# Performance work log

Measured on AMD Instinct MI355X. Metric: run time of the kernel, lower is better.

Reference implementation:

```python
import jax, jax.numpy as jnp
import numpy as np

B, T, D, K = 64, 276, 256, 8192


def setup_inputs() -> dict:
    key = jax.random.key(0)
    k1, k2 = jax.random.split(key)
    z = jax.random.normal(k1, (B, T, D), dtype=jnp.float32)
    # nn.Embedding weight init: uniform(-1/K, 1/K)
    codebook = jax.random.uniform(k2, (K, D), dtype=jnp.float32,
                                  minval=-1.0 / K, maxval=1.0 / K)
    return {"z": z, "codebook": codebook}


def reference(z, codebook):
    """Faithful port of X_BERT_VQVAE.quantize.

    z: [B, T, D] encoder output; codebook: [K, D].
    Returns (loss_vq, loss_commit, z_q [B,T,D] with straight-through, min_idx [B,T]).
    """
    bsz, t, dim = z.shape
    zf = z.reshape(bsz * t, dim)                       # (b t) d
    # pairwise sq-dist: ||z||^2 + ||c||^2 - 2 z.c  -> [(b t), K]
    d = (jnp.sum(zf * zf, axis=1, keepdims=True)
         + jnp.sum(codebook * codebook, axis=1)
         - 2.0 * zf @ codebook.T)
    min_idx = jnp.argmin(d, axis=1)                    # [(b t)]
    z_q = codebook[min_idx]                            # [(b t), D] gather
    loss_vq = jnp.mean((z_q - jax.lax.stop_gradient(zf)) ** 2)
    loss_commit = jnp.mean((zf - jax.lax.stop_gradient(z_q)) ** 2)
    # straight-through estimator
    z_q_st = zf + jax.lax.stop_gradient(z_q - zf)
    return (loss_vq, loss_commit,
            z_q_st.reshape(bsz, t, dim),
            min_idx.reshape(bsz, t))
```

## Files before the change

### kernel.cpp

```cpp
#include <hip/hip_runtime.h>
#include <hip/hip_bf16.h>

#define M_ROWS 17664
#define K_CODES 8192
#define D_DIM 256
#define N_ELEM 4521984

typedef unsigned short ushort_t;
typedef __attribute__((ext_vector_type(8))) short short8v;
typedef __attribute__((ext_vector_type(4))) float f32x4;

__device__ __forceinline__ unsigned long long umin64(unsigned long long a, unsigned long long b) { return a < b ? a : b; }

__device__ __forceinline__ unsigned long long shflxor64(unsigned long long v, int m) {
    unsigned lo = (unsigned)v, hi = (unsigned)(v >> 32);
    lo = __shfl_xor(lo, m);
    hi = __shfl_xor(hi, m);
    return ((unsigned long long)hi << 32) | lo;
}

__device__ __forceinline__ void gload16(const void* g, void* l) {
    __builtin_amdgcn_global_load_lds((const __attribute__((address_space(1))) void*)g,
                                     (__attribute__((address_space(3))) void*)l, 16, 0, 0);
}

__global__ __launch_bounds__(256) void prep_kernel(
    const float* __restrict__ Z, const float* __restrict__ CB,
    ushort_t* __restrict__ Zb, ushort_t* __restrict__ Cb,
    float* __restrict__ asum, float* __restrict__ bsum,
    float* __restrict__ loss_acc) {
    __shared__ float S[32][257];
    const int t = threadIdx.x;
    const int bid = blockIdx.x;
    const float* X; ushort_t* Xb; float* sums; int r0;
    if (bid < M_ROWS / 32) { X = Z; Xb = Zb; sums = asum; r0 = bid * 32; }
    else { X = CB; Xb = Cb; sums = bsum; r0 = (bid - M_ROWS / 32) * 32; }
    if (bid == 0 && t == 0) loss_acc[0] = 0.0f;
#pragma unroll
    for (int it = 0; it < 8; ++it) {
        int idx4 = t + it * 256;
        int row = idx4 >> 6;
        int c4 = (idx4 & 63) * 4;
        const float4 v = *(const float4*)(X + (size_t)(r0 + row) * D_DIM + c4);
        float vv[4] = {v.x, v.y, v.z, v.w};
        ushort_t h[4];
#pragma unroll
        for (int j = 0; j < 4; ++j) {
            __hip_bfloat16 b = __float2bfloat16(vv[j]);
            h[j] = *reinterpret_cast<ushort_t*>(&b);
        }
        *(ushort4*)(Xb + (size_t)(r0 + row) * D_DIM + c4) =
            make_ushort4(h[0], h[1], h[2], h[3]);
        S[row][c4 + 0] = v.x; S[row][c4 + 1] = v.y;
        S[row][c4 + 2] = v.z; S[row][c4 + 3] = v.w;
    }
    __syncthreads();
    if (t < 32) {
        float half_sum[2];
#pragma unroll
        for (int h = 0; h < 2; ++h) {
            const float* q = &S[t][h * 128];
            float acc[8];
#pragma unroll
            for (int j = 0; j < 8; ++j) acc[j] = __fmul_rn(q[j], q[j]);
            for (int i = 8; i < 128; i += 8) {
#pragma unroll
                for (int j = 0; j < 8; ++j)
                    acc[j] = __fadd_rn(acc[j], __fmul_rn(q[i + j], q[i + j]));
            }
            float s01 = __fadd_rn(acc[0], acc[1]);
            float s23 = __fadd_rn(acc[2], acc[3]);
            float s45 = __fadd_rn(acc[4], acc[5]);
            float s67 = __fadd_rn(acc[6], acc[7]);
            half_sum[h] = __fadd_rn(__fadd_rn(s01, s23), __fadd_rn(s45, s67));
        }
        sums[r0 + t] = __fadd_rn(half_sum[0], half_sum[1]);
    }
}

__global__ __launch_bounds__(256, 4) void phase1_kernel(
    const ushort_t* __restrict__ Zb,
    const ushort_t* __restrict__ Cb,
    const float* __restrict__ bsum,
    unsigned* __restrict__ blockcand) {
    __shared__ ushort_t As[8192];
    __shared__ ushort_t Bs[8192];

    const int t = threadIdx.x;
    const int wid = t >> 6, lane = t & 63;
    const int wm = wid >> 1, wn = wid & 1;

    const int bid = blockIdx.x;
    const int bn = ((bid & 7) << 3) + ((bid >> 3) & 7);
    const int bm = bid >> 6;
    const int m0 = bm * 128, n0 = bn * 128;

    f32x4 acc[4][4];
#pragma unroll
    for (int i = 0; i < 4; ++i)
#pragma unroll
        for (int jj = 0; jj < 4; ++jj) acc[i][jj] = (f32x4){0.f, 0.f, 0.f, 0.f};

    const int srow8 = t >> 3;
    const int sslot = t & 7;
    const int srcq = (sslot ^ (srow8 & 7)) * 8;
    const ushort_t* zsrc = Zb + (size_t)(m0 + srow8) * 256 + srcq;
    const ushort_t* csrc = Cb + (size_t)(n0 + srow8) * 256 + srcq;
    const int dst0 = srow8 * 64 + sslot * 8;

    const int fr = lane & 15, q = lane >> 4;
    const int ph0 = (q ^ (fr & 7)) * 8;
    const int ph1 = ((4 + q) ^ (fr & 7)) * 8;

#pragma unroll
    for (int i = 0; i < 4; ++i) {
        gload16(zsrc + (size_t)i * 8192, &As[dst0 + i * 2048]);
        gload16(csrc + (size_t)i * 8192, &Bs[dst0 + i * 2048]);
    }

#pragma unroll
    for (int c = 0; c < 4; ++c) {
        asm volatile("s_waitcnt vmcnt(0)" ::: "memory");
        __builtin_amdgcn_s_barrier();
        asm volatile("" ::: "memory");

        short8v a0[4], b0[4];
#pragma unroll
        for (int mi = 0; mi < 4; ++mi)
            a0[mi] = *(const short8v*)(&Bs[(wn * 64 + mi * 16 + fr) * 64 + ph0]);
#pragma unroll
        for (int nj = 0; nj < 4; ++nj)
            b0[nj] = *(const short8v*)(&As[(wm * 64 + nj * 16 + fr) * 64 + ph0]);
        __builtin_amdgcn_s_setprio(1);
#pragma unroll
        for (int mi = 0; mi < 4; ++mi)
#pragma unroll
            for (int nj = 0; nj < 4; ++nj)
                acc[mi][nj] = __builtin_amdgcn_mfma_f32_16x16x32_bf16(
                    a0[mi], b0[nj], acc[mi][nj], 0, 0, 0);
        __builtin_amdgcn_s_setprio(0);

        short8v a1[4], b1[4];
#pragma unroll
        for (int mi = 0; mi < 4; ++mi)
            a1[mi] = *(const short8v*)(&Bs[(wn * 64 + mi * 16 + fr) * 64 + ph1]);
#pragma unroll
        for (int nj = 0; nj < 4; ++nj)
            b1[nj] = *(const short8v*)(&As[(wm * 64 + nj * 16 + fr) * 64 + ph1]);
        asm volatile("s_waitcnt lgkmcnt(0)" ::: "memory");
        __builtin_amdgcn_sched_barrier(0);
        __builtin_amdgcn_s_barrier();
        asm volatile("" ::: "memory");

        if (c < 3) {
            const int kc = (c + 1) * 64;
#pragma unroll
            for (int i = 0; i < 4; ++i) {
                gload16(zsrc + (size_t)i * 8192 + kc, &As[dst0 + i * 2048]);
                gload16(csrc + (size_t)i * 8192 + kc, &Bs[dst0 + i * 2048]);
            }
        }

        __builtin_amdgcn_s_setprio(1);
#pragma unroll
        for (int mi = 0; mi < 4; ++mi)
#pragma unroll
            for (int nj = 0; nj < 4; ++nj)
                acc[mi][nj] = __builtin_amdgcn_mfma_f32_16x16x32_bf16(
                    a1[mi], b1[nj], acc[mi][nj], 0, 0, 0);
        __builtin_amdgcn_s_setprio(0);
    }

    unsigned* cand = (unsigned*)&As[0];
    const int colb = n0 + wn * 64 + q * 4;
    float bc16[16];
#pragma unroll
    for (int mi = 0; mi < 4; ++mi)
#pragma unroll
        for (int r = 0; r < 4; ++r)
            bc16[mi * 4 + r] = bsum[colb + mi * 16 + r];

    const float INF = __uint_as_float(0x7f800000u);
#pragma unroll
    for (int nj = 0; nj < 4; ++nj) {
        float m1 = INF, m2 = INF;
#pragma unroll
        for (int mi = 0; mi < 4; ++mi)
#pragma unroll
            for (int r = 0; r < 4; ++r) {
                float dm = __builtin_fmaf(-2.0f, acc[mi][nj][r], bc16[mi * 4 + r]);
                unsigned e = (__float_as_uint(dm) & 0xFFFFE000u) |
                             (unsigned)(colb + mi * 16 + r);
                float fe = __uint_as_float(e);
                m2 = __builtin_amdgcn_fmed3f(m1, m2, fe);
                m1 = fminf(m1, fe);
            }
#pragma unroll
        for (int s = 16; s <= 32; s <<= 1) {
            float o1 = __shfl_xor(m1, s);
            float o2 = __shfl_xor(m2, s);
            float nm2 = fminf(fmaxf(m1, o1), fminf(m2, o2));
            m1 = fminf(m1, o1);
            m2 = nm2;
        }
        if (q == 0) {
            int zr = wm * 64 + nj * 16 + fr;
            cand[zr * 9 + wn * 2 + 0] = __float_as_uint(m1);
            cand[zr * 9 + wn * 2 + 1] = __float_as_uint(m2);
        }
    }
    __syncthreads();
    if (t < 128) {
        float b1 = INF, b2 = INF;
#pragma unroll
        for (int j = 0; j < 4; ++j) {
            float f = __uint_as_float(cand[t * 9 + j]);
            b2 = __builtin_amdgcn_fmed3f(b1, b2, f);
            b1 = fminf(b1, f);
        }
        *(uint2*)(blockcand + (size_t)(m0 + t) * 128 + bn * 2) =
            make_uint2(__float_as_uint(b1), __float_as_uint(b2));
    }
}

__global__ __launch_bounds__(256) void phase2_kernel(
    const float* __restrict__ Z, const float* __restrict__ CB,
    const float* __restrict__ asum, const float* __restrict__ bsum,
    const unsigned* __restrict__ blockcand,
    float* __restrict__ out, float* __restrict__ loss_acc) {
    float* out_zq = out + 2;
    float* out_idx = out + 2 + (size_t)N_ELEM;
    const int lane = threadIdx.x & 63;
    const int w = threadIdx.x >> 6;
    const int gw = blockIdx.x * 4 + w;
    const int NW = M_ROWS / 4;
    float lsum = 0.0f;

    int row = gw;
    uint2 E = *(const uint2*)(blockcand + (size_t)row * 128 + lane * 2);
    float4 zv = *(const float4*)(Z + (size_t)row * D_DIM + lane * 4);
    float ar = asum[row];

#pragma unroll 1
    for (int it = 0; it < 4; ++it) {
        const int nrow = row + NW;
        uint2 En = E; float4 zvn = zv; float arn = ar;
        if (it < 3) {
            En = *(const uint2*)(blockcand + (size_t)nrow * 128 + lane * 2);
            zvn = *(const float4*)(Z + (size_t)nrow * D_DIM + lane * 4);
            arn = asum[nrow];
        }

        float f0 = __uint_as_float(E.x), f1 = __uint_as_float(E.y);
        float mn = fminf(f0, f1);
#pragma unroll
        for (int s = 1; s < 64; s <<= 1) mn = fminf(mn, __shfl_xor(mn, s));
        const float thr = mn + 5.0e-4f;
        unsigned long long k0m = __ballot(f0 <= thr);
        unsigned long long k1m = __ballot(f1 <= thr);

        unsigned long long best = 0xFFFFFFFFFFFFFFFFull;
        float4 bcv = make_float4(0.f, 0.f, 0.f, 0.f);

        while (k0m | k1m) {
            unsigned e;
            if (k0m) { int b = __ffsll(k0m) - 1; k0m &= k0m - 1; e = __shfl(E.x, b); }
            else     { int b = __ffsll(k1m) - 1; k1m &= k1m - 1; e = __shfl(E.y, b); }
            unsigned col = e & 8191u;
            const float4 cv = *(const float4*)(CB + (size_t)col * D_DIM + lane * 4);
            float s = __fmul_rn(zv.x, cv.x);
            s = __builtin_fmaf(zv.y, cv.y, s);
            s = __builtin_fmaf(zv.z, cv.z, s);
            s = __builtin_fmaf(zv.w, cv.w, s);
#pragma unroll
            for (int m = 1; m < 64; m <<= 1) s += __shfl_xor(s, m);
            float d = __fsub_rn(__fadd_rn(ar, bsum[col]), __fmul_rn(2.0f, s));
            unsigned long long p = ((unsigned long long)__float_as_uint(d) << 32) | col;
            if (p < best) { best = p; bcv = cv; }
        }

        unsigned wincol = (unsigned)best;
        if (lane == 0) out_idx[row] = (float)wincol;
        float d0 = __fsub_rn(bcv.x, zv.x);
        float d1 = __fsub_rn(bcv.y, zv.y);
        float d2 = __fsub_rn(bcv.z, zv.z);
        float d3 = __fsub_rn(bcv.w, zv.w);
        float2 o0 = make_float2(__fadd_rn(zv.x, d0), __fadd_rn(zv.y, d1));
        float2 o1 = make_float2(__fadd_rn(zv.z, d2), __fadd_rn(zv.w, d3));
        *(float2*)(out_zq + (size_t)row * D_DIM + lane * 4) = o0;
        *(float2*)(out_zq + (size_t)row * D_DIM + lane * 4 + 2) = o1;
        lsum += d0 * d0 + d1 * d1 + d2 * d2 + d3 * d3;

        row = nrow; E = En; zv = zvn; ar = arn;
    }

#pragma unroll
    for (int m = 1; m < 64; m <<= 1) lsum += __shfl_xor(lsum, m);
    __shared__ float red[4];
    if (lane == 0) red[w] = lsum;
    __syncthreads();
    if (threadIdx.x == 0) {
        float s = ((red[0] + red[1]) + (red[2] + red[3]));
        atomicAdd(loss_acc, s);
    }
}

__global__ void write_losses(const float* __restrict__ loss_acc,
                             float* __restrict__ out) {
    float l = __fdiv_rn(loss_acc[0], (float)N_ELEM);
    out[0] = l;
    out[1] = l;
}

#define BM 128
#define BN 128
#define BK 32
#define LDT 132

__global__ void rowsq_kernel(const float* __restrict__ X,
                             float* __restrict__ out, int rows) {
    int r = blockIdx.x * blockDim.x + threadIdx.x;
    if (r >= rows) return;
    const float* p = X + (size_t)r * D_DIM;
    float half_sum[2];
#pragma unroll
    for (int h = 0; h < 2; ++h) {
        const float* q = p + h * 128;
        float acc[8];
#pragma unroll
        for (int j = 0; j < 8; ++j) acc[j] = __fmul_rn(q[j], q[j]);
        for (int i = 8; i < 128; i += 8) {
#pragma unroll
            for (int j = 0; j < 8; ++j)
                acc[j] = __fadd_rn(acc[j], __fmul_rn(q[i + j], q[i + j]));
        }
        float s01 = __fadd_rn(acc[0], acc[1]);
        float s23 = __fadd_rn(acc[2], acc[3]);
        float s45 = __fadd_rn(acc[4], acc[5]);
        float s67 = __fadd_rn(acc[6], acc[7]);
        half_sum[h] = __fadd_rn(__fadd_rn(s01, s23), __fadd_rn(s45, s67));
    }
    out[r] = __fadd_rn(half_sum[0], half_sum[1]);
}

__global__ void init_kernel(unsigned long long* __restrict__ packed,
                            float* __restrict__ loss_acc) {
    int i = blockIdx.x * blockDim.x + threadIdx.x;
    if (i < M_ROWS) packed[i] = 0xFFFFFFFFFFFFFFFFull;
    if (i == 0) loss_acc[0] = 0.0f;
}

__global__ __launch_bounds__(256) void gemm_argmin_kernel(
    const float* __restrict__ Z, const float* __restrict__ CB,
    const float* __restrict__ asum, const float* __restrict__ bsum,
    unsigned long long* __restrict__ packed) {
    __shared__ float As[BK][LDT];
    __shared__ float Bs[BK][LDT];
    const int bid = blockIdx.x;
    const int bm = bid >> 6, bn = bid & 63;
    const int m0 = bm * BM, n0 = bn * BN;
    const int t = threadIdx.x;
    const int ty = t >> 4, tx = t & 15;
    float acc[8][8];
#pragma unroll
    for (int i = 0; i < 8; ++i)
#pragma unroll
        for (int j = 0; j < 8; ++j) acc[i][j] = 0.0f;
    for (int k0 = 0; k0 < D_DIM; k0 += BK) {
#pragma unroll
        for (int i = 0; i < 4; ++i) {
            int idx = t + i * 256;
            int row = idx >> 3, kq = idx & 7;
            const float4 av = *(const float4*)(Z + (size_t)(m0 + row) * D_DIM + k0 + kq * 4);
            As[kq * 4 + 0][row] = av.x; As[kq * 4 + 1][row] = av.y;
            As[kq * 4 + 2][row] = av.z; As[kq * 4 + 3][row] = av.w;
            const float4 bv = *(const float4*)(CB + (size_t)(n0 + row) * D_DIM + k0 + kq * 4);
            Bs[kq * 4 + 0][row] = bv.x; Bs[kq * 4 + 1][row] = bv.y;
            Bs[kq * 4 + 2][row] = bv.z; Bs[kq * 4 + 3][row] = bv.w;
        }
        __syncthreads();
#pragma unroll
        for (int k = 0; k < BK; ++k) {
            float af[8], bf[8];
            *(float4*)(af)     = *(const float4*)(&As[k][ty * 4]);
            *(float4*)(af + 4) = *(const float4*)(&As[k][64 + ty * 4]);
            *(float4*)(bf)     = *(const float4*)(&Bs[k][tx * 4]);
            *(float4*)(bf + 4) = *(const float4*)(&Bs[k][64 + tx * 4]);
#pragma unroll
            for (int i = 0; i < 8; ++i)
#pragma unroll
                for (int j = 0; j < 8; ++j)
                    acc[i][j] = __builtin_fmaf(af[i], bf[j], acc[i][j]);
        }
        __syncthreads();
    }
    float ar[8], bc[8];
    int rowIdx[8], colIdx[8];
#pragma unroll
    for (int i = 0; i < 8; ++i) {
        rowIdx[i] = (i < 4) ? (4 * ty + i) : (64 + 4 * ty + (i - 4));
        ar[i] = asum[m0 + rowIdx[i]];
    }
#pragma unroll
    for (int j = 0; j < 8; ++j) {
        colIdx[j] = (j < 4) ? (4 * tx + j) : (64 + 4 * tx + (j - 4));
        bc[j] = bsum[n0 + colIdx[j]];
    }
#pragma unroll
    for (int i = 0; i < 8; ++i) {
        unsigned long long best = 0xFFFFFFFFFFFFFFFFull;
#pragma unroll
        for (int j = 0; j < 8; ++j) {
            float ts = __fadd_rn(ar[i], bc[j]);
            float d = __fsub_rn(ts, __fmul_rn(2.0f, acc[i][j]));
            unsigned long long p = ((unsigned long long)__float_as_uint(d) << 32) |
                                   (unsigned)(n0 + colIdx[j]);
            best = (p < best) ? p : best;
        }
#pragma unroll
        for (int m = 1; m <= 8; m <<= 1) {
            unsigned long long o = shflxor64(best, m);
            best = (o < best) ? o : best;
        }
        if (tx == 0) atomicMin(&packed[m0 + rowIdx[i]], best);
    }
}

__global__ __launch_bounds__(256) void finalize_kernel(
    const float* __restrict__ Z, const float* __restrict__ CB,
    const unsigned long long* __restrict__ packed,
    float* __restrict__ out, float* __restrict__ loss_acc) {
    float* out_zq = out + 2;
    float* out_idx = out + 2 + (size_t)N_ELEM;
    const int lane = threadIdx.x & 63;
    const int wid = (blockIdx.x * blockDim.x + threadIdx.x) >> 6;
    const int nw = (gridDim.x * blockDim.x) >> 6;
    float lsum = 0.0f;
    for (int row = wid; row < M_ROWS; row += nw) {
        unsigned long long pk = packed[row];
        unsigned idx = (unsigned)(pk & 0xFFFFFFFFull);
        if (lane == 0) out_idx[row] = (float)idx;
        const float4 zv = *(const float4*)(Z + (size_t)row * D_DIM + lane * 4);
        const float4 cv = *(const float4*)(CB + (size_t)idx * D_DIM + lane * 4);
        float d0 = __fsub_rn(cv.x, zv.x);
        float d1 = __fsub_rn(cv.y, zv.y);
        float d2 = __fsub_rn(cv.z, zv.z);
        float d3 = __fsub_rn(cv.w, zv.w);
        float2 o0 = make_float2(__fadd_rn(zv.x, d0), __fadd_rn(zv.y, d1));
        float2 o1 = make_float2(__fadd_rn(zv.z, d2), __fadd_rn(zv.w, d3));
        *(float2*)(out_zq + (size_t)row * D_DIM + lane * 4) = o0;
        *(float2*)(out_zq + (size_t)row * D_DIM + lane * 4 + 2) = o1;
        lsum += d0 * d0 + d1 * d1 + d2 * d2 + d3 * d3;
    }
#pragma unroll
    for (int m = 1; m < 64; m <<= 1) lsum += __shfl_xor(lsum, m);
    __shared__ float red[4];
    if (lane == 0) red[threadIdx.x >> 6] = lsum;
    __syncthreads();
    if (threadIdx.x == 0) {
        float s = ((red[0] + red[1]) + (red[2] + red[3]));
        atomicAdd(loss_acc, s);
    }
}

extern "C" void kernel_launch(void* const* d_in, const int* in_sizes, int n_in,
                              void* d_out, int out_size, void* d_ws, size_t ws_size,
                              hipStream_t stream) {
    const float* Z = (const float*)d_in[0];
    const float* CB = (const float*)d_in[1];
    float* out = (float*)d_out;
    char* ws = (char*)d_ws;

    const size_t offZb   = 0;
    const size_t offCb   = offZb + (size_t)M_ROWS * D_DIM * 2;
    const size_t offCand = offCb + (size_t)K_CODES * D_DIM * 2;
    const size_t offAsum = offCand + (size_t)M_ROWS * 128 * 4;
    const size_t offBsum = offAsum + (size_t)M_ROWS * 4;
    const size_t offLoss = offBsum + (size_t)K_CODES * 4;
    const size_t need    = offLoss + 64;

    if (ws_size >= need) {
        ushort_t* Zb = (ushort_t*)(ws + offZb);
        ushort_t* Cb = (ushort_t*)(ws + offCb);
        unsigned* blockcand = (unsigned*)(ws + offCand);
        float* asum = (float*)(ws + offAsum);
        float* bsum = (float*)(ws + offBsum);
        float* loss_acc = (float*)(ws + offLoss);

        hipLaunchKernelGGL(prep_kernel, dim3(M_ROWS / 32 + K_CODES / 32), dim3(256),
                           0, stream, Z, CB, Zb, Cb, asum, bsum, loss_acc);
        hipLaunchKernelGGL(phase1_kernel, dim3((M_ROWS / 128) * (K_CODES / 128)),
                           dim3(256), 0, stream, Zb, Cb, bsum, blockcand);
        hipLaunchKernelGGL(phase2_kernel, dim3(M_ROWS / 16), dim3(256), 0, stream,
                           Z, CB, asum, bsum, blockcand, out, loss_acc);
        hipLaunchKernelGGL(write_losses, dim3(1), dim3(1), 0, stream, loss_acc, out);
    } else {
        float* asum = (float*)ws;
        float* bsum = (float*)(ws + (size_t)M_ROWS * 4);
        unsigned long long* packed =
            (unsigned long long*)(ws + (size_t)M_ROWS * 4 + (size_t)K_CODES * 4);
        float* loss_acc =
            (float*)(ws + (size_t)M_ROWS * 4 + (size_t)K_CODES * 4 + (size_t)M_ROWS * 8);

        hipLaunchKernelGGL(init_kernel, dim3((M_ROWS + 255) / 256), dim3(256), 0, stream,
                           packed, loss_acc);
        hipLaunchKernelGGL(rowsq_kernel, dim3((M_ROWS + 255) / 256), dim3(256), 0, stream,
                           Z, asum, M_ROWS);
        hipLaunchKernelGGL(rowsq_kernel, dim3((K_CODES + 255) / 256), dim3(256), 0, stream,
                           CB, bsum, K_CODES);
        hipLaunchKernelGGL(gemm_argmin_kernel, dim3((M_ROWS / BM) * (K_CODES / BN)),
                           dim3(256), 0, stream, Z, CB, asum, bsum, packed);
        hipLaunchKernelGGL(finalize_kernel, dim3(512), dim3(256), 0, stream,
                           Z, CB, packed, out, loss_acc);
        hipLaunchKernelGGL(write_losses, dim3(1), dim3(1), 0, stream, loss_acc, out);
    }
}
```

Before: 130.0 us.

## Make phase1 blocks persistent over three M tiles and fuse loss write

Each phase1 block now processes three consecutive 128-row Z tiles against the same codebook tile. It prefetches the next tile's first K chunk while the current tile's MFMAs run, so the per-block prologue and launch overhead are amortized and there are fewer, larger blocks. The candidate buffer moves to its own shared array so the reduction does not clobber the staging buffers. The separate write_losses kernel is dropped: the last phase2 block, found through an atomic ticket counter, writes the averaged losses. The codebook tile is reloaded for every M tile rather than kept resident, and the grid shrinks to 2944 blocks, which may reduce occupancy balance.

```diff
diff --git a/kernel.cpp b/kernel.cpp
--- a/kernel.cpp
+++ b/kernel.cpp
@@ -28,14 +28,14 @@
     const float* __restrict__ Z, const float* __restrict__ CB,
     ushort_t* __restrict__ Zb, ushort_t* __restrict__ Cb,
     float* __restrict__ asum, float* __restrict__ bsum,
-    float* __restrict__ loss_acc) {
+    float* __restrict__ loss_acc, unsigned* __restrict__ ticket) {
     __shared__ float S[32][257];
     const int t = threadIdx.x;
     const int bid = blockIdx.x;
     const float* X; ushort_t* Xb; float* sums; int r0;
     if (bid < M_ROWS / 32) { X = Z; Xb = Zb; sums = asum; r0 = bid * 32; }
     else { X = CB; Xb = Cb; sums = bsum; r0 = (bid - M_ROWS / 32) * 32; }
-    if (bid == 0 && t == 0) loss_acc[0] = 0.0f;
+    if (bid == 0 && t == 0) { loss_acc[0] = 0.0f; ticket[0] = 0u; }
 #pragma unroll
     for (int it = 0; it < 8; ++it) {
         int idx4 = t + it * 256;
@@ -85,6 +85,7 @@
     unsigned* __restrict__ blockcand) {
     __shared__ ushort_t As[8192];
     __shared__ ushort_t Bs[8192];
+    __shared__ unsigned cand[128 * 9];
 
     const int t = threadIdx.x;
     const int wid = t >> 6, lane = t & 63;
@@ -92,134 +93,152 @@
 
     const int bid = blockIdx.x;
     const int bn = ((bid & 7) << 3) + ((bid >> 3) & 7);
-    const int bm = bid >> 6;
-    const int m0 = bm * 128, n0 = bn * 128;
-
-    f32x4 acc[4][4];
-#pragma unroll
-    for (int i = 0; i < 4; ++i)
-#pragma unroll
-        for (int jj = 0; jj < 4; ++jj) acc[i][jj] = (f32x4){0.f, 0.f, 0.f, 0.f};
+    const int mg = bid >> 6;
+    const int n0 = bn * 128;
+    const int mbase = mg * 384;
 
     const int srow8 = t >> 3;
     const int sslot = t & 7;
     const int srcq = (sslot ^ (srow8 & 7)) * 8;
-    const ushort_t* zsrc = Zb + (size_t)(m0 + srow8) * 256 + srcq;
     const ushort_t* csrc = Cb + (size_t)(n0 + srow8) * 256 + srcq;
     const int dst0 = srow8 * 64 + sslot * 8;
 
     const int fr = lane & 15, q = lane >> 4;
     const int ph0 = (q ^ (fr & 7)) * 8;
     const int ph1 = ((4 + q) ^ (fr & 7)) * 8;
-
-#pragma unroll
-    for (int i = 0; i < 4; ++i) {
-        gload16(zsrc + (size_t)i * 8192, &As[dst0 + i * 2048]);
-        gload16(csrc + (size_t)i * 8192, &Bs[dst0 + i * 2048]);
-    }
-
-#pragma unroll
-    for (int c = 0; c < 4; ++c) {
-        asm volatile("s_waitcnt vmcnt(0)" ::: "memory");
-        __builtin_amdgcn_s_barrier();
-        asm volatile("" ::: "memory");
-
-        short8v a0[4], b0[4];
+    const int colb = n0 + wn * 64 + q * 4;
+    const float INF = __uint_as_float(0x7f800000u);
+
+    {
+        const ushort_t* zsrc0 = Zb + (size_t)(mbase + srow8) * 256 + srcq;
+#pragma unroll
+        for (int i = 0; i < 4; ++i) {
+            gload16(zsrc0 + (size_t)i * 8192, &As[dst0 + i * 2048]);
+            gload16(csrc + (size_t)i * 8192, &Bs[dst0 + i * 2048]);
+        }
+    }
+
+#pragma unroll 1
+    for (int m = 0; m < 3; ++m) {
+        const int m0 = mbase + m * 128;
+        const ushort_t* zsrc = Zb + (size_t)(m0 + srow8) * 256 + srcq;
+        const ushort_t* zsrcN = zsrc + 128 * 256;
+
+        f32x4 acc[4][4];
+#pragma unroll
+        for (int i = 0; i < 4; ++i)
+#pragma unroll
+            for (int jj = 0; jj < 4; ++jj) acc[i][jj] = (f32x4){0.f, 0.f, 0.f, 0.f};
+
+#pragma unroll
+        for (int c = 0; c < 4; ++c) {
+            asm volatile("s_waitcnt vmcnt(0)" ::: "memory");
+            __builtin_amdgcn_s_barrier();
+            asm volatile("" ::: "memory");
+
+            short8v a0[4], b0[4];
+#pragma unroll
+            for (int mi = 0; mi < 4; ++mi)
+                a0[mi] = *(const short8v*)(&Bs[(wn * 64 + mi * 16 + fr) * 64 + ph0]);
+#pragma unroll
+            for (int nj = 0; nj < 4; ++nj)
+                b0[nj] = *(const short8v*)(&As[(wm * 64 + nj * 16 + fr) * 64 + ph0]);
+            __builtin_amdgcn_s_setprio(1);
+#pragma unroll
+            for (int mi = 0; mi < 4; ++mi)
+#pragma unroll
+                for (int nj = 0; nj < 4; ++nj)
+                    acc[mi][nj] = __builtin_amdgcn_mfma_f32_16x16x32_bf16(
+                        a0[mi], b0[nj], acc[mi][nj], 0, 0, 0);
+            __builtin_amdgcn_s_setprio(0);
+
+            short8v a1[4], b1[4];
+#pragma unroll
+            for (int mi = 0; mi < 4; ++mi)
+                a1[mi] = *(const short8v*)(&Bs[(wn * 64 + mi * 16 + fr) * 64 + ph1]);
+#pragma unroll
+            for (int nj = 0; nj < 4; ++nj)
+                b1[nj] = *(const short8v*)(&As[(wm * 64 + nj * 16 + fr) * 64 + ph1]);
+            asm volatile("s_waitcnt lgkmcnt(0)" ::: "memory");
+            __builtin_amdgcn_sched_barrier(0);
+            __builtin_amdgcn_s_barrier();
+            asm volatile("" ::: "memory");
+
+            if (c < 3) {
+                const int kc = (c + 1) * 64;
+#pragma unroll
+                for (int i = 0; i < 4; ++i) {
+                    gload16(zsrc + (size_t)i * 8192 + kc, &As[dst0 + i * 2048]);
+                    gload16(csrc + (size_t)i * 8192 + kc, &Bs[dst0 + i * 2048]);
+                }
+            } else if (m < 2) {
+#pragma unroll
+                for (int i = 0; i < 4; ++i) {
+                    gload16(zsrcN + (size_t)i * 8192, &As[dst0 + i * 2048]);
+                    gload16(csrc + (size_t)i * 8192, &Bs[dst0 + i * 2048]);
+                }
+            }
+
+            __builtin_amdgcn_s_setprio(1);
+#pragma unroll
+            for (int mi = 0; mi < 4; ++mi)
+#pragma unroll
+                for (int nj = 0; nj < 4; ++nj)
+                    acc[mi][nj] = __builtin_amdgcn_mfma_f32_16x16x32_bf16(
+                        a1[mi], b1[nj], acc[mi][nj], 0, 0, 0);
+            __builtin_amdgcn_s_setprio(0);
+        }
+
+        float bc16[16];
 #pragma unroll
         for (int mi = 0; mi < 4; ++mi)
-            a0[mi] = *(const short8v*)(&Bs[(wn * 64 + mi * 16 + fr) * 64 + ph0]);
-#pragma unroll
-        for (int nj = 0; nj < 4; ++nj)
-            b0[nj] = *(const short8v*)(&As[(wm * 64 + nj * 16 + fr) * 64 + ph0]);
-        __builtin_amdgcn_s_setprio(1);
-#pragma unroll
-        for (int mi = 0; mi < 4; ++mi)
-#pragma unroll
-            for (int nj = 0; nj < 4; ++nj)
-                acc[mi][nj] = __builtin_amdgcn_mfma_f32_16x16x32_bf16(
-                    a0[mi], b0[nj], acc[mi][nj], 0, 0, 0);
-        __builtin_amdgcn_s_setprio(0);
-
-        short8v a1[4], b1[4];
-#pragma unroll
-        for (int mi = 0; mi < 4; ++mi)
-            a1[mi] = *(const short8v*)(&Bs[(wn * 64 + mi * 16 + fr) * 64 + ph1]);
-#pragma unroll
-        for (int nj = 0; nj < 4; ++nj)
-            b1[nj] = *(const short8v*)(&As[(wm * 64 + nj * 16 + fr) * 64 + ph1]);
+#pragma unroll
+            for (int r = 0; r < 4; ++r)
+                bc16[mi * 4 + r] = bsum[colb + mi * 16 + r];
+
+#pragma unroll
+        for (int nj = 0; nj < 4; ++nj) {
+            float m1 = INF, m2 = INF;
+#pragma unroll
+            for (int mi = 0; mi < 4; ++mi)
+#pragma unroll
+                for (int r = 0; r < 4; ++r) {
+                    float dm = __builtin_fmaf(-2.0f, acc[mi][nj][r], bc16[mi * 4 + r]);
+                    unsigned e = (__float_as_uint(dm) & 0xFFFFE000u) |
+                                 (unsigned)(colb + mi * 16 + r);
+                    float fe = __uint_as_float(e);
+                    m2 = __builtin_amdgcn_fmed3f(m1, m2, fe);
+                    m1 = fminf(m1, fe);
+                }
+#pragma unroll
+            for (int s = 16; s <= 32; s <<= 1) {
+                float o1 = __shfl_xor(m1, s);
+                float o2 = __shfl_xor(m2, s);
+                float nm2 = fminf(fmaxf(m1, o1), fminf(m2, o2));
+                m1 = fminf(m1, o1);
+                m2 = nm2;
+            }
+            if (q == 0) {
+                int zr = wm * 64 + nj * 16 + fr;
+                cand[zr * 9 + wn * 2 + 0] = __float_as_uint(m1);
+                cand[zr * 9 + wn * 2 + 1] = __float_as_uint(m2);
+            }
+        }
         asm volatile("s_waitcnt lgkmcnt(0)" ::: "memory");
         __builtin_amdgcn_sched_barrier(0);
         __builtin_amdgcn_s_barrier();
         asm volatile("" ::: "memory");
-
-        if (c < 3) {
-            const int kc = (c + 1) * 64;
-#pragma unroll
-            for (int i = 0; i < 4; ++i) {
-                gload16(zsrc + (size_t)i * 8192 + kc, &As[dst0 + i * 2048]);
-                gload16(csrc + (size_t)i * 8192 + kc, &Bs[dst0 + i * 2048]);
+        if (t < 128) {
+            float b1 = INF, b2 = INF;
+#pragma unroll
+            for (int j = 0; j < 4; ++j) {
+                float f = __uint_as_float(cand[t * 9 + j]);
+                b2 = __builtin_amdgcn_fmed3f(b1, b2, f);
+                b1 = fminf(b1, f);
             }
-        }
-
-        __builtin_amdgcn_s_setprio(1);
-#pragma unroll
-        for (int mi = 0; mi < 4; ++mi)
-#pragma unroll
-            for (int nj = 0; nj < 4; ++nj)
-                acc[mi][nj] = __builtin_amdgcn_mfma_f32_16x16x32_bf16(
-                    a1[mi], b1[nj], acc[mi][nj], 0, 0, 0);
-        __builtin_amdgcn_s_setprio(0);
-    }
-
-    unsigned* cand = (unsigned*)&As[0];
-    const int colb = n0 + wn * 64 + q * 4;
-    float bc16[16];
-#pragma unroll
-    for (int mi = 0; mi < 4; ++mi)
-#pragma unroll
-        for (int r = 0; r < 4; ++r)
-            bc16[mi * 4 + r] = bsum[colb + mi * 16 + r];
-
-    const float INF = __uint_as_float(0x7f800000u);
-#pragma unroll
-    for (int nj = 0; nj < 4; ++nj) {
-        float m1 = INF, m2 = INF;
-#pragma unroll
-        for (int mi = 0; mi < 4; ++mi)
-#pragma unroll
-            for (int r = 0; r < 4; ++r) {
-                float dm = __builtin_fmaf(-2.0f, acc[mi][nj][r], bc16[mi * 4 + r]);
-                unsigned e = (__float_as_uint(dm) & 0xFFFFE000u) |
-                             (unsigned)(colb + mi * 16 + r);
-                float fe = __uint_as_float(e);
-                m2 = __builtin_amdgcn_fmed3f(m1, m2, fe);
-                m1 = fminf(m1, fe);
-            }
-#pragma unroll
-        for (int s = 16; s <= 32; s <<= 1) {
-            float o1 = __shfl_xor(m1, s);
-            float o2 = __shfl_xor(m2, s);
-            float nm2 = fminf(fmaxf(m1, o1), fminf(m2, o2));
-            m1 = fminf(m1, o1);
-            m2 = nm2;
-        }
-        if (q == 0) {
-            int zr = wm * 64 + nj * 16 + fr;
-            cand[zr * 9 + wn * 2 + 0] = __float_as_uint(m1);
-            cand[zr * 9 + wn * 2 + 1] = __float_as_uint(m2);
-        }
-    }
-    __syncthreads();
-    if (t < 128) {
-        float b1 = INF, b2 = INF;
-#pragma unroll
-        for (int j = 0; j < 4; ++j) {
-            float f = __uint_as_float(cand[t * 9 + j]);
-            b2 = __builtin_amdgcn_fmed3f(b1, b2, f);
-            b1 = fminf(b1, f);
-        }
-        *(uint2*)(blockcand + (size_t)(m0 + t) * 128 + bn * 2) =
-            make_uint2(__float_as_uint(b1), __float_as_uint(b2));
+            *(uint2*)(blockcand + (size_t)(m0 + t) * 128 + bn * 2) =
+                make_uint2(__float_as_uint(b1), __float_as_uint(b2));
+        }
     }
 }
 
@@ -227,7 +246,8 @@
     const float* __restrict__ Z, const float* __restrict__ CB,
     const float* __restrict__ asum, const float* __restrict__ bsum,
     const unsigned* __restrict__ blockcand,
-    float* __restrict__ out, float* __restrict__ loss_acc) {
+    float* __restrict__ out, float* __restrict__ loss_acc,
+    unsigned* __restrict__ ticket) {
     float* out_zq = out + 2;
     float* out_idx = out + 2 + (size_t)N_ELEM;
     const int lane = threadIdx.x & 63;
@@ -301,7 +321,16 @@
     __syncthreads();
     if (threadIdx.x == 0) {
         float s = ((red[0] + red[1]) + (red[2] + red[3]));
-        atomicAdd(loss_acc, s);
+        float old = atomicAdd(loss_acc, s);
+        unsigned inc = 1u;
+        asm volatile("" : "+v"(inc) : "v"(old));
+        unsigned my = atomicAdd(ticket, inc);
+        if (my == gridDim.x - 1) {
+            float tot = atomicAdd(loss_acc, 0.0f);
+            float l = __fdiv_rn(tot, (float)N_ELEM);
+            out[0] = l;
+            out[1] = l;
+        }
     }
 }
 
@@ -486,14 +515,14 @@
         float* asum = (float*)(ws + offAsum);
         float* bsum = (float*)(ws + offBsum);
         float* loss_acc = (float*)(ws + offLoss);
+        unsigned* ticket = (unsigned*)(ws + offLoss + 16);
 
         hipLaunchKernelGGL(prep_kernel, dim3(M_ROWS / 32 + K_CODES / 32), dim3(256),
-                           0, stream, Z, CB, Zb, Cb, asum, bsum, loss_acc);
-        hipLaunchKernelGGL(phase1_kernel, dim3((M_ROWS / 128) * (K_CODES / 128)),
-                           dim3(256), 0, stream, Zb, Cb, bsum, blockcand);
+                           0, stream, Z, CB, Zb, Cb, asum, bsum, loss_acc, ticket);
+        hipLaunchKernelGGL(phase1_kernel, dim3(64 * 46), dim3(256), 0, stream,
+                           Zb, Cb, bsum, blockcand);
         hipLaunchKernelGGL(phase2_kernel, dim3(M_ROWS / 16), dim3(256), 0, stream,
-                           Z, CB, asum, bsum, blockcand, out, loss_acc);
-        hipLaunchKernelGGL(write_losses, dim3(1), dim3(1), 0, stream, loss_acc, out);
+                           Z, CB, asum, bsum, blockcand, out, loss_acc, ticket);
     } else {
         float* asum = (float*)ws;
         float* bsum = (float*)(ws + (size_t)M_ROWS * 4);
```

Measured after the change: 244.8 us. +88.3%, slower.
